# Performance work log

Hardware: AMD Instinct MI355X
Metric: run time of the kernel (lower is better)

Reference implementation:

```python
import jax, jax.numpy as jnp
import numpy as np

N = 50000   # nodes
E = 800000  # edges
F_IN, H, C, G = 128, 96, 16, 128  # features, hidden, classes, graphs


def gelu(x):
    return jax.nn.gelu(x, approximate=False)  # torch F.gelu default (erf)


def gcn_conv(x, W, b, src, dst, dis):
    # PyG GCNConv improved=True: A_hat = A + 2I, out = D^-1/2 A_hat D^-1/2 (x W) + b
    xw = x @ W                                   # [N, out]
    norm = dis[src] * dis[dst]                   # [E]
    msg = norm[:, None] * xw[src]                # gather + scale
    out = jax.ops.segment_sum(msg, dst, num_segments=N)
    out = out + (2.0 * dis * dis)[:, None] * xw  # self-loop with weight 2
    return out + b


def setup_inputs() -> dict:
    key = jax.random.key(0)
    ks = jax.random.split(key, 12)
    x = jax.random.normal(ks[0], (N, F_IN), dtype=jnp.float32)
    edge_index = jax.random.randint(ks[1], (2, E), 0, N, dtype=jnp.int64)
    batch = jnp.sort(jax.random.randint(ks[2], (N,), 0, G, dtype=jnp.int64))
    s = lambda fan_in: 1.0 / np.sqrt(fan_in)
    W0 = jax.random.uniform(ks[3], (F_IN, H), jnp.float32, -s(F_IN), s(F_IN))
    b0 = jnp.zeros((H,), jnp.float32)
    W1 = jax.random.uniform(ks[4], (H, H), jnp.float32, -s(H), s(H))
    b1 = jnp.zeros((H,), jnp.float32)
    W2 = jax.random.uniform(ks[5], (H, H), jnp.float32, -s(H), s(H))
    b2 = jnp.zeros((H,), jnp.float32)
    Wc1 = jax.random.uniform(ks[6], (2 * H, H), jnp.float32, -s(2 * H), s(2 * H))
    bc1 = jax.random.uniform(ks[7], (H,), jnp.float32, -s(2 * H), s(2 * H))
    Wc2 = jax.random.uniform(ks[8], (H, C), jnp.float32, -s(H), s(H))
    bc2 = jax.random.uniform(ks[9], (C,), jnp.float32, -s(H), s(H))
    return {"x": x, "edge_index": edge_index, "batch": batch,
            "W0": W0, "b0": b0, "W1": W1, "b1": b1, "W2": W2, "b2": b2,
            "Wc1": Wc1, "bc1": bc1, "Wc2": Wc2, "bc2": bc2}


def reference(x, edge_index, batch, W0, b0, W1, b1, W2, b2, Wc1, bc1, Wc2, bc2):
    src, dst = edge_index[0], edge_index[1]
    # degrees including self-loop weight 2 (improved=True)
    deg = jax.ops.segment_sum(jnp.ones((E,), x.dtype), dst, num_segments=N) + 2.0
    dis = jax.lax.rsqrt(deg)
    # layer 0: GCNConv(F_IN -> H)
    h = gcn_conv(x, W0, b0, src, dst, dis)
    # residual GCNConv layers (dropout is identity at inference)
    h = h + gcn_conv(gelu(h), W1, b1, src, dst, dis)
    h = h + gcn_conv(gelu(h), W2, b2, src, dst, dis)
    h = gelu(h)
    # global mean + max pooling per graph
    cnt = jax.ops.segment_sum(jnp.ones((N,), h.dtype), batch, num_segments=G)
    mean_p = jax.ops.segment_sum(h, batch, num_segments=G) / cnt[:, None]
    max_p = jax.ops.segment_max(h, batch, num_segments=G)
    p = jnp.concatenate([mean_p, max_p], axis=1)  # [G, 2H]
    p = p @ Wc1 + bc1
    p = gelu(p)
    return p @ Wc2 + bc2
```

## Files before the change

### kernel.cpp

```cpp
#include <hip/hip_runtime.h>
#include <hip/hip_bf16.h>

#define DEVINL __device__ __forceinline__

constexpr int N = 50000;
constexpr int E = 800000;
constexpr int F_IN = 128;
constexpr int H = 96;
constexpr int C = 16;
constexpr int G = 128;
constexpr int S = 8;
constexpr int ELLW = 64;

constexpr int OFF_W0  = 0;
constexpr int OFF_W1  = OFF_W0 + F_IN * H;
constexpr int OFF_W2  = OFF_W1 + H * H;
constexpr int OFF_WC1 = OFF_W2 + H * H;
constexpr int OFF_WC2 = OFF_WC1 + 2 * H * H;
constexpr int OFF_B0  = OFF_WC2 + H * C;
constexpr int OFF_B1  = OFF_B0 + H;
constexpr int OFF_B2  = OFF_B1 + H;
constexpr int OFF_BC1 = OFF_B2 + H;
constexpr int OFF_BC2 = OFF_BC1 + H;
constexpr int WF_TOT  = OFF_BC2 + C;

constexpr int CVB   = (WF_TOT + 255) / 256;
constexpr int GEMB  = (N + 31) / 32;
constexpr int SCB8  = 512;
constexpr int SEGSZ = (N + 7) / 8;

DEVINL float gelu_f(float x) {
    return 0.5f * x * (1.0f + erff(x * 0.70710678118654752440f));
}

DEVINL int detect_eidx_i64(const int* e) {
    int z = 0;
#pragma unroll
    for (int i = 1; i < 16; i += 2) z |= e[i];
    return z == 0;
}
DEVINL int detect_batch_i64(const int* a) {
    int z = 0;
    for (int i = 20001; i < 20032; i += 2) z |= a[i];
    return z == 0;
}
DEVINL int detect_x_f32(const unsigned short* xu) {
    int bad = 0;
    for (int i = 0; i < 128; i += 2) { int ex = (xu[i] >> 7) & 0xFF; if (ex >= 132) bad = 1; }
    return bad;
}

DEVINL unsigned pk(float a, float b) {
    __hip_bfloat16 ha = __float2bfloat16(a), hb = __float2bfloat16(b);
    unsigned short ua = *(unsigned short*)&ha, ub = *(unsigned short*)&hb;
    return (unsigned)ua | ((unsigned)ub << 16);
}
DEVINL float lo16(unsigned u) { return __uint_as_float(u << 16); }
DEVINL float hi16(unsigned u) { return __uint_as_float(u & 0xffff0000u); }

__global__ void k_prep(const void* W0, const void* W1, const void* W2,
                       const void* Wc1, const void* Wc2,
                       const void* b0, const void* b1, const void* b2,
                       const void* bc1, const void* bc2,
                       const void* x, float* __restrict__ wf) {
    int i = blockIdx.x * 256 + threadIdx.x;
    if (i >= WF_TOT) return;
    int f32 = detect_x_f32((const unsigned short*)x);
    const void* src; int j;
    if      (i < OFF_W1)  { src = W0;  j = i - OFF_W0; }
    else if (i < OFF_W2)  { src = W1;  j = i - OFF_W1; }
    else if (i < OFF_WC1) { src = W2;  j = i - OFF_W2; }
    else if (i < OFF_WC2) { src = Wc1; j = i - OFF_WC1; }
    else if (i < OFF_B0)  { src = Wc2; j = i - OFF_WC2; }
    else if (i < OFF_B1)  { src = b0;  j = i - OFF_B0; }
    else if (i < OFF_B2)  { src = b1;  j = i - OFF_B1; }
    else if (i < OFF_BC1) { src = b2;  j = i - OFF_B2; }
    else if (i < OFF_BC2) { src = bc1; j = i - OFF_BC1; }
    else                  { src = bc2; j = i - OFF_BC2; }
    wf[i] = f32 ? ((const float*)src)[j]
                : __bfloat162float(((const __hip_bfloat16*)src)[j]);
}

template<int K, int KC, bool RAW_IN, bool GELU_IN, bool SCALE_OUT>
DEVINL void gemm_tile(const void* __restrict__ inp, const float* __restrict__ Wf,
                      const float* __restrict__ dis,
                      int xf32, unsigned* __restrict__ out, int bid, int t) {
    constexpr int R = 32;
    constexpr int NC = K / KC;
    __shared__ __align__(16) float xs[KC][R + 4];
    __shared__ __align__(16) float wsh[KC * 96];
    const int r0 = bid * R;
    const int ty = t >> 4;
    const int tx = t & 15;

    float acc[4][6];
#pragma unroll
    for (int i = 0; i < 4; ++i)
#pragma unroll
        for (int j = 0; j < 6; ++j) acc[i][j] = 0.f;

    for (int c = 0; c < NC; ++c) {
        if (c) __syncthreads();
        for (int idx = t * 4; idx < KC * 96; idx += 128 * 4)
            *(float4*)&wsh[idx] = *(const float4*)&Wf[c * KC * 96 + idx];
        if (RAW_IN && !xf32) {
            for (int idx = t; idx < R * KC; idx += 128) {
                int r = idx / KC, kk = idx - r * KC;
                int row = r0 + r, k = c * KC + kk;
                float v = 0.f;
                if (row < N) v = __bfloat162float(((const __hip_bfloat16*)inp)[(size_t)row * K + k]);
                xs[kk][r] = v;
            }
        } else {
            constexpr int KC4 = KC / 4;
            for (int idx = t; idx < R * KC4; idx += 128) {
                int r = idx / KC4, k4 = (idx - r * KC4) * 4;
                int row = r0 + r, k = c * KC + k4;
                float4 v = make_float4(0.f, 0.f, 0.f, 0.f);
                if (row < N) v = *(const float4*)((const float*)inp + (size_t)row * K + k);
                if (GELU_IN) { v.x = gelu_f(v.x); v.y = gelu_f(v.y); v.z = gelu_f(v.z); v.w = gelu_f(v.w); }
                xs[k4 + 0][r] = v.x; xs[k4 + 1][r] = v.y; xs[k4 + 2][r] = v.z; xs[k4 + 3][r] = v.w;
            }
        }
        __syncthreads();

#pragma unroll 4
        for (int kk = 0; kk < KC; ++kk) {
            float4 av = *(const float4*)&xs[kk][ty * 4];
            float2 b0 = *(const float2*)&wsh[kk * 96 + tx * 6];
            float2 b1 = *(const float2*)&wsh[kk * 96 + tx * 6 + 2];
            float2 b2 = *(const float2*)&wsh[kk * 96 + tx * 6 + 4];
            float a[4] = {av.x, av.y, av.z, av.w};
            float b[6] = {b0.x, b0.y, b1.x, b1.y, b2.x, b2.y};
#pragma unroll
            for (int i = 0; i < 4; ++i)
#pragma unroll
                for (int j = 0; j < 6; ++j)
                    acc[i][j] = fmaf(a[i], b[j], acc[i][j]);
        }
    }

#pragma unroll
    for (int i = 0; i < 4; ++i) {
        int row = r0 + ty * 4 + i;
        if (row < N) {
            float d = SCALE_OUT ? dis[row] : 1.0f;
            unsigned* o = out + (size_t)row * 48 + tx * 3;
            o[0] = pk(d * acc[i][0], d * acc[i][1]);
            o[1] = pk(d * acc[i][2], d * acc[i][3]);
            o[2] = pk(d * acc[i][4], d * acc[i][5]);
        }
    }
}

__global__ __launch_bounds__(128) void k_sg(const void* __restrict__ x,
                                            const float* __restrict__ Wf,
                                            const int* __restrict__ eidx,
                                            int* __restrict__ cnt, int* __restrict__ ell,
                                            unsigned* __restrict__ outZ) {
    int b = blockIdx.x, t = threadIdx.x;
    if (b >= 8 * SCB8) {
        int gb = b - 8 * SCB8;
        if (gb >= GEMB) return;
        int xf32 = detect_x_f32((const unsigned short*)x);
        gemm_tile<F_IN, 32, true, false, false>(x, Wf, nullptr, xf32, outZ, gb, t);
        return;
    }
    int seg = b & 7, r = b >> 3;
    int i64 = detect_eidx_i64(eidx);
    constexpr int NP = E / 2;
    for (int p = r * 128 + t; p < NP; p += SCB8 * 128) {
        int d0, d1;
        if (i64) { int4 dp = *(const int4*)(eidx + 2 * E + 4 * p); d0 = dp.x; d1 = dp.z; }
        else     { int2 dp = *(const int2*)(eidx + E + 2 * p);     d0 = dp.x; d1 = dp.y; }
        bool m0 = ((unsigned)d0 / SEGSZ) == (unsigned)seg;
        bool m1 = ((unsigned)d1 / SEGSZ) == (unsigned)seg;
        if (m0 | m1) {
            int s0, s1;
            if (i64) { s0 = eidx[4 * p]; s1 = eidx[4 * p + 2]; }
            else     { s0 = eidx[2 * p]; s1 = eidx[2 * p + 1]; }
            if (m0) { int pos = atomicAdd(&cnt[d0], 1); if (pos < ELLW) ell[d0 * ELLW + pos] = s0; }
            if (m1) { int pos = atomicAdd(&cnt[d1], 1); if (pos < ELLW) ell[d1 * ELLW + pos] = s1; }
        }
    }
}

__global__ void k_dis(const int* __restrict__ cnt, float* __restrict__ dis) {
    int n = blockIdx.x * 256 + threadIdx.x;
    if (n < N) dis[n] = rsqrtf((float)min(cnt[n], ELLW) + 2.0f);
}

template<int K, int KC, bool GELU_IN>
__global__ __launch_bounds__(128) void k_gemm(const float* __restrict__ inp,
                                              const float* __restrict__ Wf,
                                              const float* __restrict__ dis,
                                              unsigned* __restrict__ out) {
    gemm_tile<K, KC, false, GELU_IN, true>(inp, Wf, dis, 1, out, blockIdx.x, threadIdx.x);
}

template<bool PRESCALED>
__global__ __launch_bounds__(256) void k_aggr(const unsigned* __restrict__ xw, const float* res,
                                              const int* __restrict__ ell, const int* __restrict__ cnt,
                                              const float* __restrict__ dis,
                                              const float* __restrict__ bias, float* __restrict__ out) {
    int wid = threadIdx.x >> 6, lane = threadIdx.x & 63;
    int n = blockIdx.x * 4 + wid;
    if (n >= N) return;
    int e0 = n * ELLW;
    int e1 = e0 + min(cnt[n], ELLW);
    int slot = lane / 12;
    int li = lane - slot * 12;
    int cp = li * 4;
    float4 A0 = make_float4(0.f, 0.f, 0.f, 0.f);
    float4 A1 = make_float4(0.f, 0.f, 0.f, 0.f);
    int eb = (slot < 5) ? (e0 + slot) : e1;
    for (; eb + 5 < e1; eb += 10) {
        int s0 = ell[eb];
        int s1 = ell[eb + 5];
        uint4 u0 = *(const uint4*)(xw + (size_t)s0 * 48 + cp);
        uint4 u1 = *(const uint4*)(xw + (size_t)s1 * 48 + cp);
        if (PRESCALED) {
            A0.x += lo16(u0.x) + lo16(u1.x); A0.y += hi16(u0.x) + hi16(u1.x);
            A0.z += lo16(u0.y) + lo16(u1.y); A0.w += hi16(u0.y) + hi16(u1.y);
            A1.x += lo16(u0.z) + lo16(u1.z); A1.y += hi16(u0.z) + hi16(u1.z);
            A1.z += lo16(u0.w) + lo16(u1.w); A1.w += hi16(u0.w) + hi16(u1.w);
        } else {
            float w0 = dis[s0], w1 = dis[s1];
            A0.x = fmaf(w0, lo16(u0.x), A0.x); A0.y = fmaf(w0, hi16(u0.x), A0.y);
            A0.z = fmaf(w0, lo16(u0.y), A0.z); A0.w = fmaf(w0, hi16(u0.y), A0.w);
            A1.x = fmaf(w0, lo16(u0.z), A1.x); A1.y = fmaf(w0, hi16(u0.z), A1.y);
            A1.z = fmaf(w0, lo16(u0.w), A1.z); A1.w = fmaf(w0, hi16(u0.w), A1.w);
            A0.x = fmaf(w1, lo16(u1.x), A0.x); A0.y = fmaf(w1, hi16(u1.x), A0.y);
            A0.z = fmaf(w1, lo16(u1.y), A0.z); A0.w = fmaf(w1, hi16(u1.y), A0.w);
            A1.x = fmaf(w1, lo16(u1.z), A1.x); A1.y = fmaf(w1, hi16(u1.z), A1.y);
            A1.z = fmaf(w1, lo16(u1.w), A1.z); A1.w = fmaf(w1, hi16(u1.w), A1.w);
        }
    }
    for (; eb < e1; eb += 5) {
        int s = ell[eb];
        uint4 u = *(const uint4*)(xw + (size_t)s * 48 + cp);
        if (PRESCALED) {
            A0.x += lo16(u.x); A0.y += hi16(u.x); A0.z += lo16(u.y); A0.w += hi16(u.y);
            A1.x += lo16(u.z); A1.y += hi16(u.z); A1.z += lo16(u.w); A1.w += hi16(u.w);
        } else {
            float w = dis[s];
            A0.x = fmaf(w, lo16(u.x), A0.x); A0.y = fmaf(w, hi16(u.x), A0.y);
            A0.z = fmaf(w, lo16(u.y), A0.z); A0.w = fmaf(w, hi16(u.y), A0.w);
            A1.x = fmaf(w, lo16(u.z), A1.x); A1.y = fmaf(w, hi16(u.z), A1.y);
            A1.z = fmaf(w, lo16(u.w), A1.z); A1.w = fmaf(w, hi16(u.w), A1.w);
        }
    }
    {
        float g0, g1, g2, g3;
        g0 = __shfl(A0.x, lane + 12); g1 = __shfl(A0.x, lane + 24); g2 = __shfl(A0.x, lane + 36); g3 = __shfl(A0.x, lane + 48);
        A0.x += g0 + g1 + g2 + g3;
        g0 = __shfl(A0.y, lane + 12); g1 = __shfl(A0.y, lane + 24); g2 = __shfl(A0.y, lane + 36); g3 = __shfl(A0.y, lane + 48);
        A0.y += g0 + g1 + g2 + g3;
        g0 = __shfl(A0.z, lane + 12); g1 = __shfl(A0.z, lane + 24); g2 = __shfl(A0.z, lane + 36); g3 = __shfl(A0.z, lane + 48);
        A0.z += g0 + g1 + g2 + g3;
        g0 = __shfl(A0.w, lane + 12); g1 = __shfl(A0.w, lane + 24); g2 = __shfl(A0.w, lane + 36); g3 = __shfl(A0.w, lane + 48);
        A0.w += g0 + g1 + g2 + g3;
        g0 = __shfl(A1.x, lane + 12); g1 = __shfl(A1.x, lane + 24); g2 = __shfl(A1.x, lane + 36); g3 = __shfl(A1.x, lane + 48);
        A1.x += g0 + g1 + g2 + g3;
        g0 = __shfl(A1.y, lane + 12); g1 = __shfl(A1.y, lane + 24); g2 = __shfl(A1.y, lane + 36); g3 = __shfl(A1.y, lane + 48);
        A1.y += g0 + g1 + g2 + g3;
        g0 = __shfl(A1.z, lane + 12); g1 = __shfl(A1.z, lane + 24); g2 = __shfl(A1.z, lane + 36); g3 = __shfl(A1.z, lane + 48);
        A1.z += g0 + g1 + g2 + g3;
        g0 = __shfl(A1.w, lane + 12); g1 = __shfl(A1.w, lane + 24); g2 = __shfl(A1.w, lane + 36); g3 = __shfl(A1.w, lane + 48);
        A1.w += g0 + g1 + g2 + g3;
    }

    if (lane < 12) {
        float dn = dis[n];
        float sc = PRESCALED ? (2.f * dn) : (2.f * dn * dn);
        int cl = li * 8;
        uint4 su = *(const uint4*)(xw + (size_t)n * 48 + cp);
        float4 sv0 = make_float4(lo16(su.x), hi16(su.x), lo16(su.y), hi16(su.y));
        float4 sv1 = make_float4(lo16(su.z), hi16(su.z), lo16(su.w), hi16(su.w));
        float4 bv0 = *(const float4*)(bias + cl);
        float4 bv1 = *(const float4*)(bias + cl + 4);
        float4 rv0 = make_float4(0.f, 0.f, 0.f, 0.f);
        float4 rv1 = make_float4(0.f, 0.f, 0.f, 0.f);
        if (res) {
            rv0 = *(const float4*)(res + (size_t)n * 96 + cl);
            rv1 = *(const float4*)(res + (size_t)n * 96 + cl + 4);
        }
        float4 o0, o1;
        o0.x = rv0.x + dn * A0.x + sc * sv0.x + bv0.x;
        o0.y = rv0.y + dn * A0.y + sc * sv0.y + bv0.y;
        o0.z = rv0.z + dn * A0.z + sc * sv0.z + bv0.z;
        o0.w = rv0.w + dn * A0.w + sc * sv0.w + bv0.w;
        o1.x = rv1.x + dn * A1.x + sc * sv1.x + bv1.x;
        o1.y = rv1.y + dn * A1.y + sc * sv1.y + bv1.y;
        o1.z = rv1.z + dn * A1.z + sc * sv1.z + bv1.z;
        o1.w = rv1.w + dn * A1.w + sc * sv1.w + bv1.w;
        *(float4*)(out + (size_t)n * 96 + cl) = o0;
        *(float4*)(out + (size_t)n * 96 + cl + 4) = o1;
    }
}

DEVINL int ld_idx(const int* a, int i64, int i) { return i64 ? a[2 * i] : a[i]; }

DEVINL int lbound_s(const int* a, int i64, int n, int key) {
    int lo = 0, hi = n;
    while (lo < hi) { int m = (lo + hi) >> 1; if (ld_idx(a, i64, m) < key) lo = m + 1; else hi = m; }
    return lo;
}

__global__ __launch_bounds__(128) void k_pool(const float* __restrict__ h, const int* __restrict__ batch,
                                              float* __restrict__ part) {
    int i64 = detect_batch_i64(batch);
    int g = blockIdx.x / S, sch = blockIdx.x % S;
    int lo = lbound_s(batch, i64, N, g), hi = lbound_s(batch, i64, N, g + 1);
    int len = hi - lo;
    int a = lo + (int)(((long long)len * sch) / S);
    int b = lo + (int)(((long long)len * (sch + 1)) / S);
    int t = threadIdx.x;
    if (t < 96) {
        float s0 = 0.f, s1 = 0.f, m0 = -INFINITY, m1 = -INFINITY;
        int n = a;
        for (; n + 1 < b; n += 2) {
            float v0 = gelu_f(h[(size_t)n * 96 + t]);
            float v1 = gelu_f(h[(size_t)(n + 1) * 96 + t]);
            s0 += v0; s1 += v1;
            m0 = fmaxf(m0, v0); m1 = fmaxf(m1, v1);
        }
        if (n < b) {
            float v = gelu_f(h[(size_t)n * 96 + t]);
            s0 += v; m0 = fmaxf(m0, v);
        }
        part[(size_t)blockIdx.x * 192 + t] = s0 + s1;
        part[(size_t)blockIdx.x * 192 + 96 + t] = fmaxf(m0, m1);
    }
}

__global__ __launch_bounds__(128) void k_cls(const float* __restrict__ part, const int* __restrict__ batch,
                                             const void* __restrict__ x,
                                             const float* __restrict__ wf, void* __restrict__ outp) {
    __shared__ float p[192];
    __shared__ float q[96];
    int i64 = detect_batch_i64(batch);
    int g = blockIdx.x, t = threadIdx.x;
    int lo = lbound_s(batch, i64, N, g), hi = lbound_s(batch, i64, N, g + 1);
    float inv = (hi > lo) ? 1.f / (float)(hi - lo) : 0.f;
    if (t < 96) {
        float sum = 0.f, mx = -INFINITY;
        for (int s = 0; s < S; ++s) {
            sum += part[(size_t)(g * S + s) * 192 + t];
            mx = fmaxf(mx, part[(size_t)(g * S + s) * 192 + 96 + t]);
        }
        p[t] = sum * inv;
        p[96 + t] = mx;
    }
    __syncthreads();
    if (t < 96) {
        float acc = wf[OFF_BC1 + t];
        const float* Wc1 = wf + OFF_WC1;
        for (int j = 0; j < 192; ++j)
            acc += p[j] * Wc1[j * 96 + t];
        q[t] = gelu_f(acc);
    }
    __syncthreads();
    if (t < 16) {
        float acc = wf[OFF_BC2 + t];
        const float* Wc2 = wf + OFF_WC2;
        for (int j = 0; j < 96; ++j)
            acc += q[j] * Wc2[j * 16 + t];
        if (detect_x_f32((const unsigned short*)x)) ((float*)outp)[g * 16 + t] = acc;
        else ((__hip_bfloat16*)outp)[g * 16 + t] = __float2bfloat16(acc);
    }
}

extern "C" void kernel_launch(void* const* d_in, const int* in_sizes, int n_in,
                              void* d_out, int out_size, void* d_ws, size_t ws_size,
                              hipStream_t stream) {
    const void* x    = d_in[0];
    const int* eidx  = (const int*)d_in[1];
    const int* batch = (const int*)d_in[2];
    (void)in_sizes; (void)n_in; (void)out_size; (void)ws_size;

    char* w = (char*)d_ws;
    size_t off = 0;
    auto take = [&](size_t bytes) { size_t o = off; off += (bytes + 511) & ~(size_t)511; return o; };
    float*    dis  = (float*)   (w + take((size_t)N * 4));
    int*      cnt  = (int*)     (w + take((size_t)N * 4));
    float*    wf   = (float*)   (w + take((size_t)WF_TOT * 4));
    int*      ell  = (int*)     (w + take((size_t)N * ELLW * 4));
    unsigned* bufA = (unsigned*)(w + take((size_t)N * 48 * 4));
    float*    bufH = (float*)   (w + take((size_t)N * 96 * 4));
    float*    part = (float*)   (w + take((size_t)G * S * 192 * 4));

    hipMemsetAsync(cnt, 0, (size_t)N * 4, stream);
    k_prep<<<CVB, 256, 0, stream>>>(d_in[3], d_in[5], d_in[7], d_in[9], d_in[11],
                                    d_in[4], d_in[6], d_in[8], d_in[10], d_in[12],
                                    x, wf);
    k_sg<<<8 * SCB8 + GEMB, 128, 0, stream>>>(x, wf + OFF_W0, eidx, cnt, ell, bufA);
    k_dis<<<(N + 255) / 256, 256, 0, stream>>>(cnt, dis);

    int aggr_grid = (N + 3) / 4;
    k_aggr<false><<<aggr_grid, 256, 0, stream>>>(bufA, nullptr, ell, cnt, dis, wf + OFF_B0, bufH);
    k_gemm<H, 48, true><<<GEMB, 128, 0, stream>>>(bufH, wf + OFF_W1, dis, bufA);
    k_aggr<true><<<aggr_grid, 256, 0, stream>>>(bufA, bufH, ell, cnt, dis, wf + OFF_B1, bufH);
    k_gemm<H, 48, true><<<GEMB, 128, 0, stream>>>(bufH, wf + OFF_W2, dis, bufA);
    k_aggr<true><<<aggr_grid, 256, 0, stream>>>(bufA, bufH, ell, cnt, dis, wf + OFF_B2, bufH);

    k_pool<<<G * S, 128, 0, stream>>>(bufH, batch, part);
    k_cls<<<G, 128, 0, stream>>>(part, batch, x, wf, d_out);
}
```

Baseline: 358.8 us.

## Single-pass edge scatter, drop dis/memset kernels, compute degree norm inline

```diff
diff --git a/kernel.cpp b/kernel.cpp
--- a/kernel.cpp
+++ b/kernel.cpp
@@ -26,8 +26,7 @@
 
 constexpr int CVB   = (WF_TOT + 255) / 256;
 constexpr int GEMB  = (N + 31) / 32;
-constexpr int SCB8  = 512;
-constexpr int SEGSZ = (N + 7) / 8;
+constexpr int SCATB = (E / 2 + 127) / 128;
 
 DEVINL float gelu_f(float x) {
     return 0.5f * x * (1.0f + erff(x * 0.70710678118654752440f));
@@ -58,12 +57,15 @@
 DEVINL float lo16(unsigned u) { return __uint_as_float(u << 16); }
 DEVINL float hi16(unsigned u) { return __uint_as_float(u & 0xffff0000u); }
 
+DEVINL float disv(int c) { return rsqrtf((float)c + 2.0f); }
+
 __global__ void k_prep(const void* W0, const void* W1, const void* W2,
                        const void* Wc1, const void* Wc2,
                        const void* b0, const void* b1, const void* b2,
                        const void* bc1, const void* bc2,
-                       const void* x, float* __restrict__ wf) {
+                       const void* x, float* __restrict__ wf, int* __restrict__ cnt) {
     int i = blockIdx.x * 256 + threadIdx.x;
+    if (i < N) cnt[i] = 0;
     if (i >= WF_TOT) return;
     int f32 = detect_x_f32((const unsigned short*)x);
     const void* src; int j;
@@ -83,7 +85,7 @@
 
 template<int K, int KC, bool RAW_IN, bool GELU_IN, bool SCALE_OUT>
 DEVINL void gemm_tile(const void* __restrict__ inp, const float* __restrict__ Wf,
-                      const float* __restrict__ dis,
+                      const int* __restrict__ cnt,
                       int xf32, unsigned* __restrict__ out, int bid, int t) {
     constexpr int R = 32;
     constexpr int NC = K / KC;
@@ -144,7 +146,7 @@
     for (int i = 0; i < 4; ++i) {
         int row = r0 + ty * 4 + i;
         if (row < N) {
-            float d = SCALE_OUT ? dis[row] : 1.0f;
+            float d = SCALE_OUT ? disv(cnt[row]) : 1.0f;
             unsigned* o = out + (size_t)row * 48 + tx * 3;
             o[0] = pk(d * acc[i][0], d * acc[i][1]);
             o[1] = pk(d * acc[i][2], d * acc[i][3]);
@@ -159,73 +161,79 @@
                                             int* __restrict__ cnt, int* __restrict__ ell,
                                             unsigned* __restrict__ outZ) {
     int b = blockIdx.x, t = threadIdx.x;
-    if (b >= 8 * SCB8) {
-        int gb = b - 8 * SCB8;
+    if (b % 3 == 0) {
+        int gb = b / 3;
         if (gb >= GEMB) return;
         int xf32 = detect_x_f32((const unsigned short*)x);
         gemm_tile<F_IN, 32, true, false, false>(x, Wf, nullptr, xf32, outZ, gb, t);
         return;
     }
-    int seg = b & 7, r = b >> 3;
+    int sb = (b / 3) * 2 + (b % 3) - 1;
+    if (sb >= SCATB) return;
+    int t2 = sb * 128 + t;
+    int e = 2 * t2;
+    if (e >= E) return;
     int i64 = detect_eidx_i64(eidx);
-    constexpr int NP = E / 2;
-    for (int p = r * 128 + t; p < NP; p += SCB8 * 128) {
-        int d0, d1;
-        if (i64) { int4 dp = *(const int4*)(eidx + 2 * E + 4 * p); d0 = dp.x; d1 = dp.z; }
-        else     { int2 dp = *(const int2*)(eidx + E + 2 * p);     d0 = dp.x; d1 = dp.y; }
-        bool m0 = ((unsigned)d0 / SEGSZ) == (unsigned)seg;
-        bool m1 = ((unsigned)d1 / SEGSZ) == (unsigned)seg;
-        if (m0 | m1) {
-            int s0, s1;
-            if (i64) { s0 = eidx[4 * p]; s1 = eidx[4 * p + 2]; }
-            else     { s0 = eidx[2 * p]; s1 = eidx[2 * p + 1]; }
-            if (m0) { int pos = atomicAdd(&cnt[d0], 1); if (pos < ELLW) ell[d0 * ELLW + pos] = s0; }
-            if (m1) { int pos = atomicAdd(&cnt[d1], 1); if (pos < ELLW) ell[d1 * ELLW + pos] = s1; }
-        }
-    }
-}
-
-__global__ void k_dis(const int* __restrict__ cnt, float* __restrict__ dis) {
-    int n = blockIdx.x * 256 + threadIdx.x;
-    if (n < N) dis[n] = rsqrtf((float)min(cnt[n], ELLW) + 2.0f);
+    int s0, s1, d0, d1;
+    if (i64) {
+        int4 sp = *(const int4*)(eidx + 4 * t2);
+        int4 dp = *(const int4*)(eidx + 2 * E + 4 * t2);
+        s0 = sp.x; s1 = sp.z; d0 = dp.x; d1 = dp.z;
+    } else {
+        int2 sp = *(const int2*)(eidx + 2 * t2);
+        int2 dp = *(const int2*)(eidx + E + 2 * t2);
+        s0 = sp.x; s1 = sp.y; d0 = dp.x; d1 = dp.y;
+    }
+    int p0 = atomicAdd(&cnt[d0], 1);
+    if (p0 < ELLW) ell[d0 * ELLW + p0] = s0;
+    if (e + 1 < E) {
+        int p1 = atomicAdd(&cnt[d1], 1);
+        if (p1 < ELLW) ell[d1 * ELLW + p1] = s1;
+    }
 }
 
 template<int K, int KC, bool GELU_IN>
 __global__ __launch_bounds__(128) void k_gemm(const float* __restrict__ inp,
                                               const float* __restrict__ Wf,
-                                              const float* __restrict__ dis,
+                                              const int* __restrict__ cnt,
                                               unsigned* __restrict__ out) {
-    gemm_tile<K, KC, false, GELU_IN, true>(inp, Wf, dis, 1, out, blockIdx.x, threadIdx.x);
+    gemm_tile<K, KC, false, GELU_IN, true>(inp, Wf, cnt, 1, out, blockIdx.x, threadIdx.x);
 }
 
 template<bool PRESCALED>
 __global__ __launch_bounds__(256) void k_aggr(const unsigned* __restrict__ xw, const float* res,
                                               const int* __restrict__ ell, const int* __restrict__ cnt,
-                                              const float* __restrict__ dis,
                                               const float* __restrict__ bias, float* __restrict__ out) {
     int wid = threadIdx.x >> 6, lane = threadIdx.x & 63;
     int n = blockIdx.x * 4 + wid;
     if (n >= N) return;
+    int cn = cnt[n];
     int e0 = n * ELLW;
-    int e1 = e0 + min(cnt[n], ELLW);
+    int e1 = e0 + min(cn, ELLW);
     int slot = lane / 12;
     int li = lane - slot * 12;
     int cp = li * 4;
     float4 A0 = make_float4(0.f, 0.f, 0.f, 0.f);
     float4 A1 = make_float4(0.f, 0.f, 0.f, 0.f);
     int eb = (slot < 5) ? (e0 + slot) : e1;
-    for (; eb + 5 < e1; eb += 10) {
+    for (; eb + 10 < e1; eb += 15) {
         int s0 = ell[eb];
         int s1 = ell[eb + 5];
+        int s2 = ell[eb + 10];
         uint4 u0 = *(const uint4*)(xw + (size_t)s0 * 48 + cp);
         uint4 u1 = *(const uint4*)(xw + (size_t)s1 * 48 + cp);
+        uint4 u2 = *(const uint4*)(xw + (size_t)s2 * 48 + cp);
         if (PRESCALED) {
-            A0.x += lo16(u0.x) + lo16(u1.x); A0.y += hi16(u0.x) + hi16(u1.x);
-            A0.z += lo16(u0.y) + lo16(u1.y); A0.w += hi16(u0.y) + hi16(u1.y);
-            A1.x += lo16(u0.z) + lo16(u1.z); A1.y += hi16(u0.z) + hi16(u1.z);
-            A1.z += lo16(u0.w) + lo16(u1.w); A1.w += hi16(u0.w) + hi16(u1.w);
+            A0.x += lo16(u0.x) + lo16(u1.x) + lo16(u2.x);
+            A0.y += hi16(u0.x) + hi16(u1.x) + hi16(u2.x);
+            A0.z += lo16(u0.y) + lo16(u1.y) + lo16(u2.y);
+            A0.w += hi16(u0.y) + hi16(u1.y) + hi16(u2.y);
+            A1.x += lo16(u0.z) + lo16(u1.z) + lo16(u2.z);
+            A1.y += hi16(u0.z) + hi16(u1.z) + hi16(u2.z);
+            A1.z += lo16(u0.w) + lo16(u1.w) + lo16(u2.w);
+            A1.w += hi16(u0.w) + hi16(u1.w) + hi16(u2.w);
         } else {
-            float w0 = dis[s0], w1 = dis[s1];
+            float w0 = disv(cnt[s0]), w1 = disv(cnt[s1]), w2 = disv(cnt[s2]);
             A0.x = fmaf(w0, lo16(u0.x), A0.x); A0.y = fmaf(w0, hi16(u0.x), A0.y);
             A0.z = fmaf(w0, lo16(u0.y), A0.z); A0.w = fmaf(w0, hi16(u0.y), A0.w);
             A1.x = fmaf(w0, lo16(u0.z), A1.x); A1.y = fmaf(w0, hi16(u0.z), A1.y);
@@ -234,6 +242,10 @@
             A0.z = fmaf(w1, lo16(u1.y), A0.z); A0.w = fmaf(w1, hi16(u1.y), A0.w);
             A1.x = fmaf(w1, lo16(u1.z), A1.x); A1.y = fmaf(w1, hi16(u1.z), A1.y);
             A1.z = fmaf(w1, lo16(u1.w), A1.z); A1.w = fmaf(w1, hi16(u1.w), A1.w);
+            A0.x = fmaf(w2, lo16(u2.x), A0.x); A0.y = fmaf(w2, hi16(u2.x), A0.y);
+            A0.z = fmaf(w2, lo16(u2.y), A0.z); A0.w = fmaf(w2, hi16(u2.y), A0.w);
+            A1.x = fmaf(w2, lo16(u2.z), A1.x); A1.y = fmaf(w2, hi16(u2.z), A1.y);
+            A1.z = fmaf(w2, lo16(u2.w), A1.z); A1.w = fmaf(w2, hi16(u2.w), A1.w);
         }
     }
     for (; eb < e1; eb += 5) {
@@ -243,7 +255,7 @@
             A0.x += lo16(u.x); A0.y += hi16(u.x); A0.z += lo16(u.y); A0.w += hi16(u.y);
             A1.x += lo16(u.z); A1.y += hi16(u.z); A1.z += lo16(u.w); A1.w += hi16(u.w);
         } else {
-            float w = dis[s];
+            float w = disv(cnt[s]);
             A0.x = fmaf(w, lo16(u.x), A0.x); A0.y = fmaf(w, hi16(u.x), A0.y);
             A0.z = fmaf(w, lo16(u.y), A0.z); A0.w = fmaf(w, hi16(u.y), A0.w);
             A1.x = fmaf(w, lo16(u.z), A1.x); A1.y = fmaf(w, hi16(u.z), A1.y);
@@ -271,7 +283,7 @@
     }
 
     if (lane < 12) {
-        float dn = dis[n];
+        float dn = disv(cn);
         float sc = PRESCALED ? (2.f * dn) : (2.f * dn * dn);
         int cl = li * 8;
         uint4 su = *(const uint4*)(xw + (size_t)n * 48 + cp);
@@ -382,7 +394,6 @@
     char* w = (char*)d_ws;
     size_t off = 0;
     auto take = [&](size_t bytes) { size_t o = off; off += (bytes + 511) & ~(size_t)511; return o; };
-    float*    dis  = (float*)   (w + take((size_t)N * 4));
     int*      cnt  = (int*)     (w + take((size_t)N * 4));
     float*    wf   = (float*)   (w + take((size_t)WF_TOT * 4));
     int*      ell  = (int*)     (w + take((size_t)N * ELLW * 4));
@@ -390,19 +401,17 @@
     float*    bufH = (float*)   (w + take((size_t)N * 96 * 4));
     float*    part = (float*)   (w + take((size_t)G * S * 192 * 4));
 
-    hipMemsetAsync(cnt, 0, (size_t)N * 4, stream);
     k_prep<<<CVB, 256, 0, stream>>>(d_in[3], d_in[5], d_in[7], d_in[9], d_in[11],
                                     d_in[4], d_in[6], d_in[8], d_in[10], d_in[12],
-                                    x, wf);
-    k_sg<<<8 * SCB8 + GEMB, 128, 0, stream>>>(x, wf + OFF_W0, eidx, cnt, ell, bufA);
-    k_dis<<<(N + 255) / 256, 256, 0, stream>>>(cnt, dis);
+                                    x, wf, cnt);
+    k_sg<<<3 * GEMB, 128, 0, stream>>>(x, wf + OFF_W0, eidx, cnt, ell, bufA);
 
     int aggr_grid = (N + 3) / 4;
-    k_aggr<false><<<aggr_grid, 256, 0, stream>>>(bufA, nullptr, ell, cnt, dis, wf + OFF_B0, bufH);
-    k_gemm<H, 48, true><<<GEMB, 128, 0, stream>>>(bufH, wf + OFF_W1, dis, bufA);
-    k_aggr<true><<<aggr_grid, 256, 0, stream>>>(bufA, bufH, ell, cnt, dis, wf + OFF_B1, bufH);
-    k_gemm<H, 48, true><<<GEMB, 128, 0, stream>>>(bufH, wf + OFF_W2, dis, bufA);
-    k_aggr<true><<<aggr_grid, 256, 0, stream>>>(bufA, bufH, ell, cnt, dis, wf + OFF_B2, bufH);
+    k_aggr<false><<<aggr_grid, 256, 0, stream>>>(bufA, nullptr, ell, cnt, wf + OFF_B0, bufH);
+    k_gemm<H, 48, true><<<GEMB, 128, 0, stream>>>(bufH, wf + OFF_W1, cnt, bufA);
+    k_aggr<true><<<aggr_grid, 256, 0, stream>>>(bufA, bufH, ell, cnt, wf + OFF_B1, bufH);
+    k_gemm<H, 48, true><<<GEMB, 128, 0, stream>>>(bufH, wf + OFF_W2, cnt, bufA);
+    k_aggr<true><<<aggr_grid, 256, 0, stream>>>(bufA, bufH, ell, cnt, wf + OFF_B2, bufH);
 
     k_pool<<<G * S, 128, 0, stream>>>(bufH, batch, part);
     k_cls<<<G, 128, 0, stream>>>(part, batch, x, wf, d_out);
```

Result: no change. 352.8 us (-1.7%).
